# Performance work log

Hardware: AMD Instinct MI355X
Metric: run time of the kernel (lower is better)

The kernel has to match this reference:

```python
import jax, jax.numpy as jnp
import numpy as np

L, ND, ED, AD = 2, 128, 64, 64
N, E, A, G = 50000, 300000, 600000, 16
EPS = 1e-5


def _graph_norm(h, batch, num_graphs, w, b):
    # PyG LayerNorm(mode='graph'): scalar mean/var over all nodes*features per graph.
    F = h.shape[-1]
    cnt = jax.ops.segment_sum(jnp.ones(h.shape[0], h.dtype), batch, num_segments=num_graphs)
    norm = jnp.maximum(cnt, 1.0) * F  # [G]
    mean = (jax.ops.segment_sum(h, batch, num_segments=num_graphs).sum(-1) / norm)[batch][:, None]
    hc = h - mean
    var = (jax.ops.segment_sum(hc * hc, batch, num_segments=num_graphs).sum(-1) / norm)
    out = hc * jax.lax.rsqrt(var + EPS)[batch][:, None]
    return out * w + b


def setup_inputs() -> dict:
    key = jax.random.key(0)
    ks = jax.random.split(key, 24)

    def lin(k, fi, fo):
        return jax.random.normal(k, (L, fi, fo), jnp.float32) / jnp.sqrt(float(fi))

    inp = {
        "x": jax.random.normal(ks[0], (N, ND), jnp.float32),
        "edge_attr": jax.random.normal(ks[1], (E, ED), jnp.float32),
        "angle_attr": jax.random.normal(ks[2], (A, AD), jnp.float32),
        # node_edge_mlp: [2*ND+ED -> ED], plain linear (plain_last=True)
        "W_ne": lin(ks[3], 2 * ND + ED, ED), "b_ne": jnp.zeros((L, ED), jnp.float32),
        "g_e": jnp.ones((L, ED), jnp.float32), "be_e": jnp.zeros((L, ED), jnp.float32),
        # edge_angle_mlp: [2*ED+AD -> AD]
        "W_ea": lin(ks[4], 2 * ED + AD, AD), "b_ea": jnp.zeros((L, AD), jnp.float32),
        "g_a": jnp.ones((L, AD), jnp.float32), "be_a": jnp.zeros((L, AD), jnp.float32),
        # edge_graph_mp message net: [2*ED+AD -> ED]
        "W_emp": lin(ks[5], 2 * ED + AD, ED), "b_emp": jnp.zeros((L, ED), jnp.float32),
        "g_emp": jnp.ones((L, ED), jnp.float32), "be_emp": jnp.zeros((L, ED), jnp.float32),
        # node_graph_mp message net: [2*ND+ED -> ND]
        "W_nmp": lin(ks[6], 2 * ND + ED, ND), "b_nmp": jnp.zeros((L, ND), jnp.float32),
        "g_nmp": jnp.ones((L, ND), jnp.float32), "be_nmp": jnp.zeros((L, ND), jnp.float32),
        "node_batch": jnp.sort(jax.random.randint(ks[7], (N,), 0, G)),
        "edge_index": jax.random.randint(ks[8], (2, E), 0, N),
        "edge_batch": jnp.sort(jax.random.randint(ks[9], (E,), 0, G)),
        "threebody_index": jax.random.randint(ks[10], (2, A), 0, E),
        "angle_batch": jnp.sort(jax.random.randint(ks[11], (A,), 0, G)),
        "num_graphs": G,
    }
    return inp


def reference(x, edge_attr, angle_attr,
              W_ne, b_ne, g_e, be_e,
              W_ea, b_ea, g_a, be_a,
              W_emp, b_emp, g_emp, be_emp,
              W_nmp, b_nmp, g_nmp, be_nmp,
              node_batch, edge_index, edge_batch,
              threebody_index, angle_batch, num_graphs):
    src_e, dst_e = edge_index[0], edge_index[1]
    src_t, dst_t = threebody_index[0], threebody_index[1]
    n_nodes, n_edges = x.shape[0], edge_attr.shape[0]
    for i in range(W_ne.shape[0]):
        # node-pair -> edge update + residual + graph norm
        ecat = jnp.concatenate([x[src_e], x[dst_e], edge_attr], axis=-1)
        edge_attr = edge_attr + ecat @ W_ne[i] + b_ne[i]
        edge_attr = _graph_norm(edge_attr, edge_batch, num_graphs, g_e[i], be_e[i])
        # edge-pair -> angle update + residual + graph norm
        acat = jnp.concatenate([edge_attr[src_t], edge_attr[dst_t], angle_attr], axis=-1)
        angle_attr = angle_attr + acat @ W_ea[i] + b_ea[i]
        angle_attr = _graph_norm(angle_attr, angle_batch, num_graphs, g_a[i], be_a[i])
        # edge_graph_mp: angle-mediated message passing over edges
        mcat = jnp.concatenate([edge_attr[src_t], edge_attr[dst_t], angle_attr], axis=-1)
        msg = jax.nn.relu(mcat @ W_emp[i] + b_emp[i])
        agg = jax.ops.segment_sum(msg, dst_t, num_segments=n_edges)
        edge_attr = _graph_norm(edge_attr + agg, edge_batch, num_graphs, g_emp[i], be_emp[i])
        # node_graph_mp: edge-mediated message passing over nodes
        ncat = jnp.concatenate([x[src_e], x[dst_e], edge_attr], axis=-1)
        nmsg = jax.nn.relu(ncat @ W_nmp[i] + b_nmp[i])
        nagg = jax.ops.segment_sum(nmsg, dst_e, num_segments=n_nodes)
        x = _graph_norm(x + nagg, node_batch, num_graphs, g_nmp[i], be_nmp[i])
    return x
```

## Files before the change

### kernel.cpp

```cpp
#include <hip/hip_runtime.h>

typedef __attribute__((ext_vector_type(8))) short bf16x8_t;
typedef __attribute__((ext_vector_type(4))) short bf16x4_t;
typedef __attribute__((ext_vector_type(4))) float f32x4_t;

constexpr int NG = 16;
constexpr float EPS = 1e-5f;

__device__ inline unsigned short f2bf(float f) {
  unsigned u = __builtin_bit_cast(unsigned, f);
  u += 0x7FFFu + ((u >> 16) & 1u);
  return (unsigned short)(u >> 16);
}
__device__ inline float bf2f(unsigned short u) {
  unsigned x = ((unsigned)u) << 16;
  return __builtin_bit_cast(float, x);
}

__global__ __launch_bounds__(256) void k_dense_x(
    const float* __restrict__ x,
    const unsigned short* __restrict__ WtNE,
    const unsigned short* __restrict__ WtNM,
    unsigned short* __restrict__ P, int nN)
{
  int gw = (int)((blockIdx.x * 256u + threadIdx.x) >> 6);
  int ntile = nN >> 4;
  if (gw >= ntile) return;
  int lane = threadIdx.x & 63;
  int colb = lane & 15;
  int ko = (lane >> 4) << 3;
  int rowb = (lane >> 4) << 2;
  int row = (gw << 4) + colb;
  const float* xr = x + (size_t)row * 128;
  f32x4_t a1[4] = {}, a2[4] = {}, a3[8] = {}, a4[8] = {};
#pragma unroll
  for (int c = 0; c < 4; ++c) {
    float4 f0 = *(const float4*)(xr + c * 32 + ko);
    float4 f1 = *(const float4*)(xr + c * 32 + ko + 4);
    float vv[8] = {f0.x,f0.y,f0.z,f0.w,f1.x,f1.y,f1.z,f1.w};
    bf16x8_t a;
#pragma unroll
    for (int k = 0; k < 8; ++k) a[k] = (short)f2bf(vv[k]);
#pragma unroll
    for (int nb = 0; nb < 4; ++nb) {
      bf16x8_t b1 = *(const bf16x8_t*)(WtNE + (size_t)(nb * 16 + colb) * 320 + c * 32 + ko);
      a1[nb] = __builtin_amdgcn_mfma_f32_16x16x32_bf16(a, b1, a1[nb], 0, 0, 0);
      bf16x8_t b2 = *(const bf16x8_t*)(WtNE + (size_t)(nb * 16 + colb) * 320 + (c + 4) * 32 + ko);
      a2[nb] = __builtin_amdgcn_mfma_f32_16x16x32_bf16(a, b2, a2[nb], 0, 0, 0);
    }
#pragma unroll
    for (int nb = 0; nb < 8; ++nb) {
      bf16x8_t b3 = *(const bf16x8_t*)(WtNM + (size_t)(nb * 16 + colb) * 320 + c * 32 + ko);
      a3[nb] = __builtin_amdgcn_mfma_f32_16x16x32_bf16(a, b3, a3[nb], 0, 0, 0);
      bf16x8_t b4 = *(const bf16x8_t*)(WtNM + (size_t)(nb * 16 + colb) * 320 + (c + 4) * 32 + ko);
      a4[nb] = __builtin_amdgcn_mfma_f32_16x16x32_bf16(a, b4, a4[nb], 0, 0, 0);
    }
  }
#pragma unroll
  for (int r = 0; r < 4; ++r) {
    size_t ro = (size_t)((gw << 4) + rowb + r) * 384;
    bf16x4_t t1, t2;
#pragma unroll
    for (int nb = 0; nb < 4; ++nb) { t1[nb] = (short)f2bf(a1[nb][r]); t2[nb] = (short)f2bf(a2[nb][r]); }
    *(bf16x4_t*)(P + ro + colb * 4) = t1;
    *(bf16x4_t*)(P + ro + 64 + colb * 4) = t2;
    bf16x8_t t3, t4;
#pragma unroll
    for (int nb = 0; nb < 8; ++nb) { t3[nb] = (short)f2bf(a3[nb][r]); t4[nb] = (short)f2bf(a4[nb][r]); }
    *(bf16x8_t*)(P + ro + 128 + colb * 8) = t3;
    *(bf16x8_t*)(P + ro + 256 + colb * 8) = t4;
  }
}

__global__ __launch_bounds__(256) void k_edge(
    const unsigned short* __restrict__ P, const float* e_in, float* e_out,
    const int* __restrict__ ei, const int* __restrict__ ebatch,
    const unsigned short* __restrict__ Wt,
    const float* __restrict__ bias,
    const float* __restrict__ afA, const float* __restrict__ afB,
    float* __restrict__ gs1, float* __restrict__ gs2,
    unsigned short* __restrict__ pn, int nE)
{
  __shared__ float lA[1024], lB[1024];
  __shared__ float ls1[NG], ls2[NG];
  for (int i = threadIdx.x; i < 1024; i += 256) { lA[i] = afA[i]; lB[i] = afB[i]; }
  if (threadIdx.x < NG) { ls1[threadIdx.x] = 0.f; ls2[threadIdx.x] = 0.f; }
  __syncthreads();
  int gw = (int)((blockIdx.x * 256u + threadIdx.x) >> 6);
  int ntile = nE >> 4;
  bool act = gw < ntile;
  int lane = threadIdx.x & 63;
  int colb = lane & 15;
  int ko = (lane >> 4) << 3;
  int rowb = (lane >> 4) << 2;
  float sr[4] = {0.f,0.f,0.f,0.f}, ssr[4] = {0.f,0.f,0.f,0.f};
  if (act) {
    int sI[4], dI[4];
#pragma unroll
    for (int r = 0; r < 4; ++r) {
      int e_r = (gw << 4) + rowb + r;
      sI[r] = ei[e_r]; dI[r] = ei[nE + e_r];
    }
    bf16x4_t g1[4], g2[4]; bf16x8_t g3[4], g4[4];
#pragma unroll
    for (int r = 0; r < 4; ++r) {
      g1[r] = *(const bf16x4_t*)(P + (size_t)sI[r] * 384 + colb * 4);
      g2[r] = *(const bf16x4_t*)(P + (size_t)dI[r] * 384 + 64 + colb * 4);
      g3[r] = *(const bf16x8_t*)(P + (size_t)sI[r] * 384 + 128 + colb * 8);
      g4[r] = *(const bf16x8_t*)(P + (size_t)dI[r] * 384 + 256 + colb * 8);
    }
    int row = (gw << 4) + colb;
    int ge = ebatch[row];
    const float* er = e_in + (size_t)row * 64;
    f32x4_t acc[4] = {};
#pragma unroll
    for (int c2 = 0; c2 < 2; ++c2) {
      int fb = c2 * 32 + ko;
      float4 f0 = *(const float4*)(er + fb);
      float4 f1 = *(const float4*)(er + fb + 4);
      float vv[8] = {f0.x,f0.y,f0.z,f0.w,f1.x,f1.y,f1.z,f1.w};
      bf16x8_t a;
#pragma unroll
      for (int k = 0; k < 8; ++k) a[k] = (short)f2bf(vv[k] * lA[ge*64 + fb + k] + lB[ge*64 + fb + k]);
#pragma unroll
      for (int nb = 0; nb < 4; ++nb) {
        bf16x8_t b = *(const bf16x8_t*)(Wt + (size_t)(nb * 16 + colb) * 320 + (8 + c2) * 32 + ko);
        acc[nb] = __builtin_amdgcn_mfma_f32_16x16x32_bf16(a, b, acc[nb], 0, 0, 0);
      }
    }
#pragma unroll
    for (int r = 0; r < 4; ++r) {
      int e_ = (gw << 4) + rowb + r;
      int gr = ebatch[e_];
#pragma unroll
      for (int nb = 0; nb < 4; ++nb) {
        int col = nb * 16 + colb;
        size_t off = (size_t)e_ * 64 + col;
        float vv = e_in[off] * lA[gr*64 + col] + lB[gr*64 + col] + bias[col]
                 + acc[nb][r] + bf2f((unsigned short)g1[r][nb]) + bf2f((unsigned short)g2[r][nb]);
        e_out[off] = vv;
        sr[r] += vv; ssr[r] += vv * vv;
      }
      bf16x8_t pv;
#pragma unroll
      for (int k = 0; k < 8; ++k)
        pv[k] = (short)f2bf(bf2f((unsigned short)g3[r][k]) + bf2f((unsigned short)g4[r][k]));
      *(bf16x8_t*)(pn + (size_t)e_ * 128 + colb * 8) = pv;
    }
  }
#pragma unroll
  for (int m = 1; m <= 8; m <<= 1)
#pragma unroll
    for (int r = 0; r < 4; ++r) { sr[r] += __shfl_xor(sr[r], m); ssr[r] += __shfl_xor(ssr[r], m); }
  if (act && colb == 0) {
#pragma unroll
    for (int r = 0; r < 4; ++r) {
      int g = ebatch[(gw << 4) + rowb + r];
      atomicAdd(&ls1[g], sr[r]); atomicAdd(&ls2[g], ssr[r]);
    }
  }
  __syncthreads();
  if (threadIdx.x < NG) {
    atomicAdd(&gs1[threadIdx.x], ls1[threadIdx.x]);
    atomicAdd(&gs2[threadIdx.x], ls2[threadIdx.x]);
  }
}

__global__ __launch_bounds__(256) void k_fin_nmp(
    const float* __restrict__ e, const int* __restrict__ ebatch,
    const unsigned short* __restrict__ Wt,
    const float* __restrict__ bias,
    const float* __restrict__ afEA, const float* __restrict__ afEB,
    const unsigned short* __restrict__ pn,
    unsigned short* __restrict__ msg, int nE)
{
  __shared__ float lEA[1024], lEB[1024];
  for (int i = threadIdx.x; i < 1024; i += 256) { lEA[i] = afEA[i]; lEB[i] = afEB[i]; }
  __syncthreads();
  int gw = (int)((blockIdx.x * 256u + threadIdx.x) >> 6);
  int ntile = nE >> 4;
  if (gw >= ntile) return;
  int lane = threadIdx.x & 63;
  int colb = lane & 15;
  int ko = (lane >> 4) << 3;
  int rowb = (lane >> 4) << 2;
  int row = (gw << 4) + colb;
  int ge = ebatch[row];
  const float* er = e + (size_t)row * 64;
  f32x4_t acc[8] = {};
#pragma unroll
  for (int c2 = 0; c2 < 2; ++c2) {
    int fb = c2 * 32 + ko;
    float4 f0 = *(const float4*)(er + fb);
    float4 f1 = *(const float4*)(er + fb + 4);
    float vv[8] = {f0.x,f0.y,f0.z,f0.w,f1.x,f1.y,f1.z,f1.w};
    bf16x8_t a;
#pragma unroll
    for (int k = 0; k < 8; ++k) a[k] = (short)f2bf(vv[k] * lEA[ge*64 + fb + k] + lEB[ge*64 + fb + k]);
#pragma unroll
    for (int nb = 0; nb < 8; ++nb) {
      bf16x8_t b = *(const bf16x8_t*)(Wt + (size_t)(nb * 16 + colb) * 320 + (8 + c2) * 32 + ko);
      acc[nb] = __builtin_amdgcn_mfma_f32_16x16x32_bf16(a, b, acc[nb], 0, 0, 0);
    }
  }
#pragma unroll
  for (int r = 0; r < 4; ++r) {
    int e_ = (gw << 4) + rowb + r;
    bf16x8_t p8 = *(const bf16x8_t*)(pn + (size_t)e_ * 128 + colb * 8);
#pragma unroll
    for (int nb = 0; nb < 8; ++nb) {
      int col = nb * 16 + colb;
      float v = fmaxf(acc[nb][r] + bf2f((unsigned short)p8[nb]) + bias[col], 0.f);
      msg[(size_t)e_ * 128 + col] = f2bf(v);
    }
  }
}

__global__ __launch_bounds__(256) void k_mm_angle(
    const unsigned short* __restrict__ eB1, const float* a_in, float* a_out,
    const int* __restrict__ ti, const int* __restrict__ abatch,
    const unsigned short* __restrict__ Wt, const float* __restrict__ bias,
    const float* __restrict__ afAA, const float* __restrict__ afAB,
    float* __restrict__ gs1, float* __restrict__ gs2, int nA)
{
  __shared__ float lAA[1024], lAB[1024];
  __shared__ float ls1[NG], ls2[NG];
  for (int i = threadIdx.x; i < 1024; i += 256) { lAA[i] = afAA[i]; lAB[i] = afAB[i]; }
  if (threadIdx.x < NG) { ls1[threadIdx.x] = 0.f; ls2[threadIdx.x] = 0.f; }
  __syncthreads();
  int gw = (int)((blockIdx.x * 256u + threadIdx.x) >> 6);
  int ntile = nA >> 4;
  bool act = gw < ntile;
  int lane = threadIdx.x & 63;
  int colb = lane & 15;
  int ko = (lane >> 4) << 3;
  int rowb = (lane >> 4) << 2;
  float sr[4] = {0.f,0.f,0.f,0.f}, ssr[4] = {0.f,0.f,0.f,0.f};
  if (act) {
    int row = (gw << 4) + colb;
    int s = ti[row], d = ti[nA + row];
    int ga = abatch[row];
    const unsigned short* es = eB1 + (size_t)s * 64;
    const unsigned short* ed = eB1 + (size_t)d * 64;
    const float* ar = a_in + (size_t)row * 64;
    f32x4_t acc[4] = {};
#pragma unroll
    for (int c = 0; c < 6; ++c) {
      bf16x8_t a;
      if (c < 4) {
        const unsigned short* bp = (c < 2) ? es + c * 32 : ed + (c - 2) * 32;
        a = *(const bf16x8_t*)(bp + ko);
      } else {
        int fb = (c - 4) * 32 + ko;
        float4 f0 = *(const float4*)(ar + fb);
        float4 f1 = *(const float4*)(ar + fb + 4);
        float vv[8] = {f0.x,f0.y,f0.z,f0.w,f1.x,f1.y,f1.z,f1.w};
#pragma unroll
        for (int k = 0; k < 8; ++k) a[k] = (short)f2bf(vv[k] * lAA[ga*64 + fb + k] + lAB[ga*64 + fb + k]);
      }
#pragma unroll
      for (int nb = 0; nb < 4; ++nb) {
        bf16x8_t b = *(const bf16x8_t*)(Wt + (size_t)(nb * 16 + colb) * 192 + c * 32 + ko);
        acc[nb] = __builtin_amdgcn_mfma_f32_16x16x32_bf16(a, b, acc[nb], 0, 0, 0);
      }
    }
#pragma unroll
    for (int r = 0; r < 4; ++r) {
      int a_ = (gw << 4) + rowb + r;
      int gr = abatch[a_];
#pragma unroll
      for (int nb = 0; nb < 4; ++nb) {
        int col = nb * 16 + colb;
        size_t off = (size_t)a_ * 64 + col;
        float vv = a_in[off] * lAA[gr*64 + col] + lAB[gr*64 + col] + bias[col] + acc[nb][r];
        a_out[off] = vv;
        sr[r] += vv; ssr[r] += vv * vv;
      }
    }
  }
#pragma unroll
  for (int m = 1; m <= 8; m <<= 1)
#pragma unroll
    for (int r = 0; r < 4; ++r) { sr[r] += __shfl_xor(sr[r], m); ssr[r] += __shfl_xor(ssr[r], m); }
  if (act && colb == 0) {
#pragma unroll
    for (int r = 0; r < 4; ++r) {
      int g = abatch[(gw << 4) + rowb + r];
      atomicAdd(&ls1[g], sr[r]); atomicAdd(&ls2[g], ssr[r]);
    }
  }
  __syncthreads();
  if (threadIdx.x < NG) {
    atomicAdd(&gs1[threadIdx.x], ls1[threadIdx.x]);
    atomicAdd(&gs2[threadIdx.x], ls2[threadIdx.x]);
  }
}

__global__ __launch_bounds__(256) void k_mm_emp(
    const unsigned short* __restrict__ eB1, const float* __restrict__ a_,
    const int* __restrict__ ti, const int* __restrict__ abatch,
    const unsigned short* __restrict__ Wt, const float* __restrict__ bias,
    const float* __restrict__ afAA, const float* __restrict__ afAB,
    unsigned short* __restrict__ msg, int nA)
{
  __shared__ float lAA[1024], lAB[1024];
  for (int i = threadIdx.x; i < 1024; i += 256) { lAA[i] = afAA[i]; lAB[i] = afAB[i]; }
  __syncthreads();
  int gw = (int)((blockIdx.x * 256u + threadIdx.x) >> 6);
  int ntile = nA >> 4;
  if (gw >= ntile) return;
  int lane = threadIdx.x & 63;
  int colb = lane & 15;
  int ko = (lane >> 4) << 3;
  int rowb = (lane >> 4) << 2;
  int row = (gw << 4) + colb;
  int s = ti[row], d = ti[nA + row];
  int ga = abatch[row];
  const unsigned short* es = eB1 + (size_t)s * 64;
  const unsigned short* ed = eB1 + (size_t)d * 64;
  const float* ar = a_ + (size_t)row * 64;
  f32x4_t acc[4] = {};
#pragma unroll
  for (int c = 0; c < 6; ++c) {
    bf16x8_t a;
    if (c < 4) {
      const unsigned short* bp = (c < 2) ? es + c * 32 : ed + (c - 2) * 32;
      a = *(const bf16x8_t*)(bp + ko);
    } else {
      int fb = (c - 4) * 32 + ko;
      float4 f0 = *(const float4*)(ar + fb);
      float4 f1 = *(const float4*)(ar + fb + 4);
      float vv[8] = {f0.x,f0.y,f0.z,f0.w,f1.x,f1.y,f1.z,f1.w};
#pragma unroll
      for (int k = 0; k < 8; ++k) a[k] = (short)f2bf(vv[k] * lAA[ga*64 + fb + k] + lAB[ga*64 + fb + k]);
    }
#pragma unroll
    for (int nb = 0; nb < 4; ++nb) {
      bf16x8_t b = *(const bf16x8_t*)(Wt + (size_t)(nb * 16 + colb) * 192 + c * 32 + ko);
      acc[nb] = __builtin_amdgcn_mfma_f32_16x16x32_bf16(a, b, acc[nb], 0, 0, 0);
    }
  }
#pragma unroll
  for (int r = 0; r < 4; ++r) {
    int a_idx = (gw << 4) + rowb + r;
#pragma unroll
    for (int nb = 0; nb < 4; ++nb) {
      int col = nb * 16 + colb;
      float v = fmaxf(acc[nb][r] + bias[col], 0.f);
      msg[(size_t)a_idx * 64 + col] = f2bf(v);
    }
  }
}

__global__ __launch_bounds__(256) void k_red_e(
    const unsigned short* __restrict__ msg, const float* e_in, float* e_out,
    const int* __restrict__ ptr, const int* __restrict__ perm,
    const int* __restrict__ ebatch,
    const float* __restrict__ afA, const float* __restrict__ afB,
    float* __restrict__ gs1, float* __restrict__ gs2, int nE)
{
  __shared__ float lA[1024], lB[1024], ls1[NG], ls2[NG];
  for (int i = threadIdx.x; i < 1024; i += 256) { lA[i] = afA[i]; lB[i] = afB[i]; }
  if (threadIdx.x < NG) { ls1[threadIdx.x] = 0.f; ls2[threadIdx.x] = 0.f; }
  __syncthreads();
  int lane = threadIdx.x & 63;
  int wv = (int)((blockIdx.x * 256u + threadIdx.x) >> 6);
  int nw = (int)((gridDim.x * 256u) >> 6);
  for (int eidx = wv; eidx < nE; eidx += nw) {
    int p0 = ptr[eidx], p1 = ptr[eidx + 1];
    float sum = 0.f;
    for (int j = p0; j < p1; ++j) {
      int aidx = perm[j];
      sum += bf2f(msg[(size_t)aidx * 64 + lane]);
    }
    int g = ebatch[eidx];
    size_t off = (size_t)eidx * 64 + lane;
    float v = e_in[off] * lA[g*64 + lane] + lB[g*64 + lane] + sum;
    e_out[off] = v;
    float s = v, ss = v * v;
#pragma unroll
    for (int m = 1; m < 64; m <<= 1) { s += __shfl_xor(s, m); ss += __shfl_xor(ss, m); }
    if (lane == 0) { atomicAdd(&ls1[g], s); atomicAdd(&ls2[g], ss); }
  }
  __syncthreads();
  if (threadIdx.x < NG) {
    atomicAdd(&gs1[threadIdx.x], ls1[threadIdx.x]);
    atomicAdd(&gs2[threadIdx.x], ls2[threadIdx.x]);
  }
}

__global__ __launch_bounds__(256) void k_red_n(
    const unsigned short* __restrict__ msg, const float* x_in, float* out,
    const int* __restrict__ ptr, const int* __restrict__ perm,
    const int* __restrict__ nbatch,
    float* __restrict__ gs1, float* __restrict__ gs2, int nN)
{
  __shared__ float ls1[NG], ls2[NG];
  if (threadIdx.x < NG) { ls1[threadIdx.x] = 0.f; ls2[threadIdx.x] = 0.f; }
  __syncthreads();
  int lane = threadIdx.x & 63;
  int wv = (int)((blockIdx.x * 256u + threadIdx.x) >> 6);
  int nw = (int)((gridDim.x * 256u) >> 6);
  for (int n = wv; n < nN; n += nw) {
    int p0 = ptr[n], p1 = ptr[n + 1];
    float s0 = 0.f, s1v = 0.f;
    for (int j = p0; j < p1; ++j) {
      int e = perm[j];
      unsigned u = *(const unsigned*)(msg + (size_t)e * 128 + lane * 2);
      s0 += bf2f((unsigned short)(u & 0xffffu));
      s1v += bf2f((unsigned short)(u >> 16));
    }
    size_t off = (size_t)n * 128 + lane * 2;
    float h0 = x_in[off] + s0, h1 = x_in[off + 1] + s1v;
    out[off] = h0; out[off + 1] = h1;
    float s = h0 + h1, ss = h0 * h0 + h1 * h1;
#pragma unroll
    for (int m = 1; m < 64; m <<= 1) { s += __shfl_xor(s, m); ss += __shfl_xor(ss, m); }
    if (lane == 0) { int g = nbatch[n]; atomicAdd(&ls1[g], s); atomicAdd(&ls2[g], ss); }
  }
  __syncthreads();
  if (threadIdx.x < NG) {
    atomicAdd(&gs1[threadIdx.x], ls1[threadIdx.x]);
    atomicAdd(&gs2[threadIdx.x], ls2[threadIdx.x]);
  }
}

__global__ __launch_bounds__(256) void k_mkaff(
    const float* __restrict__ s1, const float* __restrict__ s2,
    const float* __restrict__ cnt, int F,
    const float* __restrict__ w, const float* __restrict__ b,
    float* __restrict__ A, float* __restrict__ B)
{
  int idx = blockIdx.x * 256 + threadIdx.x;
  if (idx >= NG * F) return;
  int g = idx / F, f = idx - g * F;
  float norm = fmaxf(cnt[g], 1.f) * (float)F;
  float m = s1[g] / norm;
  float var = s2[g] / norm - m * m;
  float inv = rsqrtf(var + EPS);
  float a = inv * w[f];
  A[idx] = a;
  B[idx] = b[f] - m * a;
}

__global__ __launch_bounds__(256) void k_idaff(float* __restrict__ A, float* __restrict__ B, int n)
{
  int idx = blockIdx.x * 256 + threadIdx.x;
  if (idx < n) { A[idx] = 1.f; B[idx] = 0.f; }
}

__global__ __launch_bounds__(256) void k_norm_ebf(
    const float* __restrict__ e, const int* __restrict__ ebatch,
    const float* __restrict__ afA, const float* __restrict__ afB,
    unsigned short* __restrict__ eB, int nE)
{
  int total = nE * 8;
  int stride = gridDim.x * 256;
  for (int idx = blockIdx.x * 256 + threadIdx.x; idx < total; idx += stride) {
    int row = idx >> 3, q = (idx & 7) * 8;
    int g = ebatch[row];
    const float* er = e + (size_t)row * 64 + q;
    float4 f0 = *(const float4*)er;
    float4 f1 = *(const float4*)(er + 4);
    float vv[8] = {f0.x,f0.y,f0.z,f0.w,f1.x,f1.y,f1.z,f1.w};
    bf16x8_t o;
#pragma unroll
    for (int k = 0; k < 8; ++k) o[k] = (short)f2bf(vv[k] * afA[g*64 + q + k] + afB[g*64 + q + k]);
    *(bf16x8_t*)(eB + (size_t)row * 64 + q) = o;
  }
}

__global__ __launch_bounds__(256) void k_apply(
    float* h, const int* __restrict__ batch,
    const float* __restrict__ A, const float* __restrict__ B, int nN)
{
  int total = nN * 16;
  int stride = gridDim.x * 256;
  for (int idx = blockIdx.x * 256 + threadIdx.x; idx < total; idx += stride) {
    int row = idx >> 4, q = (idx & 15) * 8;
    int g = batch[row];
    float* hp = h + (size_t)row * 128 + q;
    float4 f0 = *(const float4*)hp;
    float4 f1 = *(const float4*)(hp + 4);
    float vv[8] = {f0.x,f0.y,f0.z,f0.w,f1.x,f1.y,f1.z,f1.w};
#pragma unroll
    for (int k = 0; k < 8; ++k) vv[k] = vv[k] * A[(g << 7) + q + k] + B[(g << 7) + q + k];
    float4 g0 = {vv[0],vv[1],vv[2],vv[3]}, g1 = {vv[4],vv[5],vv[6],vv[7]};
    *(float4*)hp = g0;
    *(float4*)(hp + 4) = g1;
  }
}

__global__ __launch_bounds__(256) void k_count(
    const int* __restrict__ batch, int n, float* __restrict__ cnt)
{
  __shared__ float lc[NG];
  if (threadIdx.x < NG) lc[threadIdx.x] = 0.f;
  __syncthreads();
  for (int i = blockIdx.x * 256 + threadIdx.x; i < n; i += gridDim.x * 256)
    atomicAdd(&lc[batch[i]], 1.f);
  __syncthreads();
  if (threadIdx.x < NG) atomicAdd(&cnt[threadIdx.x], lc[threadIdx.x]);
}

__global__ __launch_bounds__(256) void k_hist(
    const int* __restrict__ dst, int n, int* __restrict__ cnt)
{
  for (int i = blockIdx.x * 256 + threadIdx.x; i < n; i += gridDim.x * 256)
    atomicAdd(&cnt[dst[i]], 1);
}

__global__ __launch_bounds__(256) void k_scan1(
    const int* __restrict__ in, int* __restrict__ out, int* __restrict__ bsum, int n)
{
  __shared__ int wtot[4];
  int tid = threadIdx.x, lane = tid & 63, wid = tid >> 6;
  int base = blockIdx.x * 1024 + tid * 4;
  int v[4];
#pragma unroll
  for (int k = 0; k < 4; ++k) v[k] = (base + k < n) ? in[base + k] : 0;
  int tsum = v[0] + v[1] + v[2] + v[3];
  int incl = tsum;
#pragma unroll
  for (int off = 1; off < 64; off <<= 1) {
    int up = __shfl_up(incl, off);
    if (lane >= off) incl += up;
  }
  if (lane == 63) wtot[wid] = incl;
  __syncthreads();
  if (tid == 0) {
    int r = 0;
#pragma unroll
    for (int w2 = 0; w2 < 4; ++w2) { int t = wtot[w2]; wtot[w2] = r; r += t; }
    bsum[blockIdx.x] = r;
  }
  __syncthreads();
  int excl = wtot[wid] + incl - tsum;
#pragma unroll
  for (int k = 0; k < 4; ++k) {
    if (base + k < n) out[base + k] = excl;
    excl += v[k];
  }
}

__global__ __launch_bounds__(256) void k_scan2(int* __restrict__ bsum, int nb, int* __restrict__ total_out)
{
  __shared__ int wtot[4];
  int tid = threadIdx.x, lane = tid & 63, wid = tid >> 6;
  int base = tid * 4;
  int v[4];
#pragma unroll
  for (int k = 0; k < 4; ++k) v[k] = (base + k < nb) ? bsum[base + k] : 0;
  int tsum = v[0] + v[1] + v[2] + v[3];
  int incl = tsum;
#pragma unroll
  for (int off = 1; off < 64; off <<= 1) {
    int up = __shfl_up(incl, off);
    if (lane >= off) incl += up;
  }
  if (lane == 63) wtot[wid] = incl;
  __syncthreads();
  if (tid == 0) {
    int r = 0;
#pragma unroll
    for (int w2 = 0; w2 < 4; ++w2) { int t = wtot[w2]; wtot[w2] = r; r += t; }
    *total_out = r;
  }
  __syncthreads();
  int excl = wtot[wid] + incl - tsum;
#pragma unroll
  for (int k = 0; k < 4; ++k) {
    if (base + k < nb) bsum[base + k] = excl;
    excl += v[k];
  }
}

__global__ __launch_bounds__(256) void k_scan3(
    int* __restrict__ ptr, int* __restrict__ cur, const int* __restrict__ bsum, int n)
{
  for (int i = blockIdx.x * 256 + threadIdx.x; i < n; i += gridDim.x * 256) {
    int v = ptr[i] + bsum[i >> 10];
    ptr[i] = v; cur[i] = v;
  }
}

__global__ __launch_bounds__(256) void k_scatter(
    const int* __restrict__ dst, int* __restrict__ cur, int* __restrict__ perm, int n)
{
  for (int i = blockIdx.x * 256 + threadIdx.x; i < n; i += gridDim.x * 256) {
    int d = dst[i];
    int p = atomicAdd(&cur[d], 1);
    perm[p] = i;
  }
}

__global__ __launch_bounds__(256) void k_wt(
    const float* __restrict__ W, unsigned short* __restrict__ Wt, int K, int NO)
{
  int idx = blockIdx.x * 256 + threadIdx.x;
  if (idx >= K * NO) return;
  int k = idx / NO, j = idx - k * NO;
  Wt[(size_t)j * K + k] = f2bf(W[idx]);
}

extern "C" void kernel_launch(void* const* d_in, const int* in_sizes, int n_in,
                              void* d_out, int out_size, void* d_ws, size_t ws_size,
                              hipStream_t stream)
{
  const float* x0    = (const float*)d_in[0];
  const float* e0    = (const float*)d_in[1];
  const float* a0    = (const float*)d_in[2];
  const float* W_ne  = (const float*)d_in[3];
  const float* b_ne  = (const float*)d_in[4];
  const float* g_e   = (const float*)d_in[5];
  const float* be_e  = (const float*)d_in[6];
  const float* W_ea  = (const float*)d_in[7];
  const float* b_ea  = (const float*)d_in[8];
  const float* g_a   = (const float*)d_in[9];
  const float* be_a  = (const float*)d_in[10];
  const float* W_emp = (const float*)d_in[11];
  const float* b_emp = (const float*)d_in[12];
  const float* g_emp = (const float*)d_in[13];
  const float* be_emp= (const float*)d_in[14];
  const float* W_nmp = (const float*)d_in[15];
  const float* b_nmp = (const float*)d_in[16];
  const float* g_nmp = (const float*)d_in[17];
  const float* be_nmp= (const float*)d_in[18];
  const int* node_batch  = (const int*)d_in[19];
  const int* edge_index  = (const int*)d_in[20];
  const int* edge_batch  = (const int*)d_in[21];
  const int* tb_index    = (const int*)d_in[22];
  const int* angle_batch = (const int*)d_in[23];

  const int N = in_sizes[0] / 128;
  const int E = in_sizes[1] / 64;
  const int A = in_sizes[2] / 64;

  char* wsp = (char*)d_ws;
  auto alloc = [&](size_t bytes) { char* p = wsp; wsp += (bytes + 255) & ~(size_t)255; return p; };
  float*          eA     = (float*)alloc((size_t)E * 64 * 4);
  float*          aA     = (float*)alloc((size_t)A * 64 * 4);
  unsigned short* msg    = (unsigned short*)alloc((size_t)A * 64 * 2);
  unsigned short* pn     = (unsigned short*)alloc((size_t)E * 128 * 2);
  unsigned short* eB1    = (unsigned short*)alloc((size_t)E * 64 * 2);
  int* ptr_n  = (int*)alloc((size_t)(N + 1) * 4);
  int* cur_n  = (int*)alloc((size_t)N * 4);
  int* perm_n = (int*)alloc((size_t)E * 4);
  int* ptr_e  = (int*)alloc((size_t)(E + 1) * 4);
  int* cur_e  = (int*)alloc((size_t)E * 4);
  int* perm_e = (int*)alloc((size_t)A * 4);
  int* bsum   = (int*)alloc(4096 * 4);
  float* stats = (float*)alloc(5 * NG * 4);
  float* s1    = stats;
  float* s2    = stats + NG;
  float* cnt_n = stats + 2 * NG;
  float* cnt_e = stats + 3 * NG;
  float* cnt_a = stats + 4 * NG;
  float* afE_idA = (float*)alloc(1024 * 4); float* afE_idB = (float*)alloc(1024 * 4);
  float* afA_idA = (float*)alloc(1024 * 4); float* afA_idB = (float*)alloc(1024 * 4);
  float* afE1A   = (float*)alloc(1024 * 4); float* afE1B   = (float*)alloc(1024 * 4);
  float* afE2A   = (float*)alloc(1024 * 4); float* afE2B   = (float*)alloc(1024 * 4);
  float* afA1A   = (float*)alloc(1024 * 4); float* afA1B   = (float*)alloc(1024 * 4);
  float* afXA    = (float*)alloc(2048 * 4); float* afXB    = (float*)alloc(2048 * 4);
  unsigned short* wt_ne  = (unsigned short*)alloc((size_t)2 * 320 * 64 * 2);
  unsigned short* wt_ea  = (unsigned short*)alloc((size_t)2 * 192 * 64 * 2);
  unsigned short* wt_emp = (unsigned short*)alloc((size_t)2 * 192 * 64 * 2);
  unsigned short* wt_nmp = (unsigned short*)alloc((size_t)2 * 320 * 128 * 2);

  unsigned short* P = msg;
  float* x_out = (float*)d_out;

  for (int i = 0; i < 2; ++i) {
    k_wt<<<(320*64 + 255)/256, 256, 0, stream>>>(W_ne  + (size_t)i*320*64,  wt_ne  + (size_t)i*320*64,  320, 64);
    k_wt<<<(192*64 + 255)/256, 256, 0, stream>>>(W_ea  + (size_t)i*192*64,  wt_ea  + (size_t)i*192*64,  192, 64);
    k_wt<<<(192*64 + 255)/256, 256, 0, stream>>>(W_emp + (size_t)i*192*64,  wt_emp + (size_t)i*192*64,  192, 64);
    k_wt<<<(320*128 + 255)/256, 256, 0, stream>>>(W_nmp + (size_t)i*320*128, wt_nmp + (size_t)i*320*128, 320, 128);
  }
  hipMemsetAsync(stats, 0, 5 * NG * 4, stream);
  k_count<<<512, 256, 0, stream>>>(node_batch, N, cnt_n);
  k_count<<<512, 256, 0, stream>>>(edge_batch, E, cnt_e);
  k_count<<<512, 256, 0, stream>>>(angle_batch, A, cnt_a);
  k_idaff<<<4, 256, 0, stream>>>(afE_idA, afE_idB, 1024);
  k_idaff<<<4, 256, 0, stream>>>(afA_idA, afA_idB, 1024);

  hipMemsetAsync(cur_n, 0, (size_t)N * 4, stream);
  hipMemsetAsync(cur_e, 0, (size_t)E * 4, stream);
  k_hist<<<1024, 256, 0, stream>>>(edge_index + E, E, cur_n);
  k_hist<<<1024, 256, 0, stream>>>(tb_index + A, A, cur_e);
  int nbN = (N + 1023) / 1024, nbE = (E + 1023) / 1024;
  k_scan1<<<nbN, 256, 0, stream>>>(cur_n, ptr_n, bsum, N);
  k_scan2<<<1, 256, 0, stream>>>(bsum, nbN, ptr_n + N);
  k_scan3<<<1024, 256, 0, stream>>>(ptr_n, cur_n, bsum, N);
  k_scatter<<<1024, 256, 0, stream>>>(edge_index + E, cur_n, perm_n, E);
  k_scan1<<<nbE, 256, 0, stream>>>(cur_e, ptr_e, bsum, E);
  k_scan2<<<1, 256, 0, stream>>>(bsum, nbE, ptr_e + E);
  k_scan3<<<1024, 256, 0, stream>>>(ptr_e, cur_e, bsum, E);
  k_scatter<<<1024, 256, 0, stream>>>(tb_index + A, cur_e, perm_e, A);

  const float* x_cur = x0;
  int blkE = (E / 16 + 3) / 4;
  int blkA = (A / 16 + 3) / 4;
  int blkN = (N / 16 + 3) / 4;

  for (int i = 0; i < 2; ++i) {
    const float* e_in  = (i == 0) ? e0 : eA;
    const float* a_in  = (i == 0) ? a0 : aA;
    const float* fEinA = (i == 0) ? afE_idA : afE2A;
    const float* fEinB = (i == 0) ? afE_idB : afE2B;
    const float* fAinA = (i == 0) ? afA_idA : afA1A;
    const float* fAinB = (i == 0) ? afA_idB : afA1B;

    k_dense_x<<<blkN, 256, 0, stream>>>(x_cur, wt_ne + (size_t)i*320*64,
                                        wt_nmp + (size_t)i*320*128, P, N);

    hipMemsetAsync(s1, 0, 2 * NG * 4, stream);
    k_edge<<<blkE, 256, 0, stream>>>(P, e_in, eA, edge_index, edge_batch,
                                     wt_ne + (size_t)i*320*64, b_ne + i*64,
                                     fEinA, fEinB, s1, s2, pn, E);
    k_mkaff<<<4, 256, 0, stream>>>(s1, s2, cnt_e, 64, g_e + i*64, be_e + i*64, afE1A, afE1B);
    k_norm_ebf<<<2048, 256, 0, stream>>>(eA, edge_batch, afE1A, afE1B, eB1, E);

    hipMemsetAsync(s1, 0, 2 * NG * 4, stream);
    k_mm_angle<<<blkA, 256, 0, stream>>>(eB1, a_in, aA, tb_index, angle_batch,
                                         wt_ea + (size_t)i*192*64, b_ea + i*64,
                                         fAinA, fAinB, s1, s2, A);
    k_mkaff<<<4, 256, 0, stream>>>(s1, s2, cnt_a, 64, g_a + i*64, be_a + i*64, afA1A, afA1B);

    k_mm_emp<<<blkA, 256, 0, stream>>>(eB1, aA, tb_index, angle_batch,
                                       wt_emp + (size_t)i*192*64, b_emp + i*64,
                                       afA1A, afA1B, msg, A);
    hipMemsetAsync(s1, 0, 2 * NG * 4, stream);
    k_red_e<<<2048, 256, 0, stream>>>(msg, eA, eA, ptr_e, perm_e, edge_batch,
                                      afE1A, afE1B, s1, s2, E);
    k_mkaff<<<4, 256, 0, stream>>>(s1, s2, cnt_e, 64, g_emp + i*64, be_emp + i*64, afE2A, afE2B);

    k_fin_nmp<<<blkE, 256, 0, stream>>>(eA, edge_batch, wt_nmp + (size_t)i*320*128,
                                        b_nmp + i*128, afE2A, afE2B, pn, msg, E);
    hipMemsetAsync(s1, 0, 2 * NG * 4, stream);
    k_red_n<<<2048, 256, 0, stream>>>(msg, x_cur, x_out, ptr_n, perm_n, node_batch,
                                      s1, s2, N);
    k_mkaff<<<8, 256, 0, stream>>>(s1, s2, cnt_n, 128, g_nmp + i*128, be_nmp + i*128, afXA, afXB);
    k_apply<<<2048, 256, 0, stream>>>(x_out, node_batch, afXA, afXB, N);

    x_cur = x_out;
  }
}
```

Baseline: 1.866 ms.

## Precompute per-edge emp projections and gather them in the angle kernel

Splits the edge-angle message matmul by linearity. The edge-feature parts of W_emp are multiplied once per edge (300k rows) into a bf16 PE buffer, instead of once per angle (600k rows). The angle kernel gathers the two projected halves, sums them into the msg buffer, and k_fin_emp adds only the angle-feature projection. This roughly halves the emp matmul work on the edge part and shrinks the gather, but adds an extra workspace buffer plus an intermediate bf16 rounding step, and falls back to the old path if the workspace is too small.

```diff
diff --git a/kernel.cpp b/kernel.cpp
--- a/kernel.cpp
+++ b/kernel.cpp
@@ -72,6 +72,43 @@
   }
 }
 
+__global__ __launch_bounds__(256) void k_dense_e(
+    const unsigned short* __restrict__ eB1,
+    const unsigned short* __restrict__ WtP,
+    unsigned short* __restrict__ PE, int nE)
+{
+  int gw = (int)((blockIdx.x * 256u + threadIdx.x) >> 6);
+  int ntile = nE >> 4;
+  if (gw >= ntile) return;
+  int lane = threadIdx.x & 63;
+  int colb = lane & 15;
+  int ko = (lane >> 4) << 3;
+  int rowb = (lane >> 4) << 2;
+  int row = (gw << 4) + colb;
+  const unsigned short* er = eB1 + (size_t)row * 64;
+  f32x4_t a3[4] = {}, a4[4] = {};
+#pragma unroll
+  for (int c2 = 0; c2 < 2; ++c2) {
+    bf16x8_t a = *(const bf16x8_t*)(er + c2 * 32 + ko);
+#pragma unroll
+    for (int nb = 0; nb < 4; ++nb) {
+      bf16x8_t b3 = *(const bf16x8_t*)(WtP + (size_t)(nb * 16 + colb) * 192 + c2 * 32 + ko);
+      a3[nb] = __builtin_amdgcn_mfma_f32_16x16x32_bf16(a, b3, a3[nb], 0, 0, 0);
+      bf16x8_t b4 = *(const bf16x8_t*)(WtP + (size_t)(nb * 16 + colb) * 192 + 64 + c2 * 32 + ko);
+      a4[nb] = __builtin_amdgcn_mfma_f32_16x16x32_bf16(a, b4, a4[nb], 0, 0, 0);
+    }
+  }
+#pragma unroll
+  for (int r = 0; r < 4; ++r) {
+    size_t ro = (size_t)((gw << 4) + rowb + r) * 128;
+    bf16x4_t t3, t4;
+#pragma unroll
+    for (int nb = 0; nb < 4; ++nb) { t3[nb] = (short)f2bf(a3[nb][r]); t4[nb] = (short)f2bf(a4[nb][r]); }
+    *(bf16x4_t*)(PE + ro + colb * 4) = t3;
+    *(bf16x4_t*)(PE + ro + 64 + colb * 4) = t4;
+  }
+}
+
 __global__ __launch_bounds__(256) void k_edge(
     const unsigned short* __restrict__ P, const float* e_in, float* e_out,
     const int* __restrict__ ei, const int* __restrict__ ebatch,
@@ -163,6 +200,157 @@
   if (threadIdx.x < NG) {
     atomicAdd(&gs1[threadIdx.x], ls1[threadIdx.x]);
     atomicAdd(&gs2[threadIdx.x], ls2[threadIdx.x]);
+  }
+}
+
+__global__ __launch_bounds__(256) void k_angle(
+    const unsigned short* __restrict__ eB1, const unsigned short* __restrict__ PE,
+    const float* a_in, float* a_out,
+    const int* __restrict__ ti, const int* __restrict__ abatch,
+    const unsigned short* __restrict__ Wt, const float* __restrict__ bias,
+    const float* __restrict__ afAA, const float* __restrict__ afAB,
+    float* __restrict__ gs1, float* __restrict__ gs2,
+    unsigned short* __restrict__ pe, int nA)
+{
+  __shared__ float lAA[1024], lAB[1024];
+  __shared__ float ls1[NG], ls2[NG];
+  for (int i = threadIdx.x; i < 1024; i += 256) { lAA[i] = afAA[i]; lAB[i] = afAB[i]; }
+  if (threadIdx.x < NG) { ls1[threadIdx.x] = 0.f; ls2[threadIdx.x] = 0.f; }
+  __syncthreads();
+  int gw = (int)((blockIdx.x * 256u + threadIdx.x) >> 6);
+  int ntile = nA >> 4;
+  bool act = gw < ntile;
+  int lane = threadIdx.x & 63;
+  int colb = lane & 15;
+  int ko = (lane >> 4) << 3;
+  int rowb = (lane >> 4) << 2;
+  float sr[4] = {0.f,0.f,0.f,0.f}, ssr[4] = {0.f,0.f,0.f,0.f};
+  if (act) {
+    int sI[4], dI[4];
+#pragma unroll
+    for (int r = 0; r < 4; ++r) {
+      int a_r = (gw << 4) + rowb + r;
+      sI[r] = ti[a_r]; dI[r] = ti[nA + a_r];
+    }
+    bf16x4_t g3[4], g4[4];
+#pragma unroll
+    for (int r = 0; r < 4; ++r) {
+      g3[r] = *(const bf16x4_t*)(PE + (size_t)sI[r] * 128 + colb * 4);
+      g4[r] = *(const bf16x4_t*)(PE + (size_t)dI[r] * 128 + 64 + colb * 4);
+    }
+    int row = (gw << 4) + colb;
+    int s = ti[row], d = ti[nA + row];
+    int ga = abatch[row];
+    const unsigned short* es = eB1 + (size_t)s * 64;
+    const unsigned short* ed = eB1 + (size_t)d * 64;
+    const float* ar = a_in + (size_t)row * 64;
+    f32x4_t acc[4] = {};
+#pragma unroll
+    for (int c = 0; c < 6; ++c) {
+      bf16x8_t a;
+      if (c < 4) {
+        const unsigned short* bp = (c < 2) ? es + c * 32 : ed + (c - 2) * 32;
+        a = *(const bf16x8_t*)(bp + ko);
+      } else {
+        int fb = (c - 4) * 32 + ko;
+        float4 f0 = *(const float4*)(ar + fb);
+        float4 f1 = *(const float4*)(ar + fb + 4);
+        float vv[8] = {f0.x,f0.y,f0.z,f0.w,f1.x,f1.y,f1.z,f1.w};
+#pragma unroll
+        for (int k = 0; k < 8; ++k) a[k] = (short)f2bf(vv[k] * lAA[ga*64 + fb + k] + lAB[ga*64 + fb + k]);
+      }
+#pragma unroll
+      for (int nb = 0; nb < 4; ++nb) {
+        bf16x8_t b = *(const bf16x8_t*)(Wt + (size_t)(nb * 16 + colb) * 192 + c * 32 + ko);
+        acc[nb] = __builtin_amdgcn_mfma_f32_16x16x32_bf16(a, b, acc[nb], 0, 0, 0);
+      }
+    }
+#pragma unroll
+    for (int r = 0; r < 4; ++r) {
+      int a_ = (gw << 4) + rowb + r;
+      int gr = abatch[a_];
+#pragma unroll
+      for (int nb = 0; nb < 4; ++nb) {
+        int col = nb * 16 + colb;
+        size_t off = (size_t)a_ * 64 + col;
+        float vv = a_in[off] * lAA[gr*64 + col] + lAB[gr*64 + col] + bias[col] + acc[nb][r];
+        a_out[off] = vv;
+        sr[r] += vv; ssr[r] += vv * vv;
+      }
+      bf16x4_t pv;
+#pragma unroll
+      for (int nb = 0; nb < 4; ++nb)
+        pv[nb] = (short)f2bf(bf2f((unsigned short)g3[r][nb]) + bf2f((unsigned short)g4[r][nb]));
+      *(bf16x4_t*)(pe + (size_t)a_ * 64 + colb * 4) = pv;
+    }
+  }
+#pragma unroll
+  for (int m = 1; m <= 8; m <<= 1)
+#pragma unroll
+    for (int r = 0; r < 4; ++r) { sr[r] += __shfl_xor(sr[r], m); ssr[r] += __shfl_xor(ssr[r], m); }
+  if (act && colb == 0) {
+#pragma unroll
+    for (int r = 0; r < 4; ++r) {
+      int g = abatch[(gw << 4) + rowb + r];
+      atomicAdd(&ls1[g], sr[r]); atomicAdd(&ls2[g], ssr[r]);
+    }
+  }
+  __syncthreads();
+  if (threadIdx.x < NG) {
+    atomicAdd(&gs1[threadIdx.x], ls1[threadIdx.x]);
+    atomicAdd(&gs2[threadIdx.x], ls2[threadIdx.x]);
+  }
+}
+
+__global__ __launch_bounds__(256) void k_fin_emp(
+    const float* __restrict__ a_, const int* __restrict__ abatch,
+    const unsigned short* __restrict__ Wt,
+    const float* __restrict__ bias,
+    const float* __restrict__ afAA, const float* __restrict__ afAB,
+    unsigned short* __restrict__ msg, int nA)
+{
+  __shared__ float lAA[1024], lAB[1024];
+  for (int i = threadIdx.x; i < 1024; i += 256) { lAA[i] = afAA[i]; lAB[i] = afAB[i]; }
+  __syncthreads();
+  int gw = (int)((blockIdx.x * 256u + threadIdx.x) >> 6);
+  int ntile = nA >> 4;
+  if (gw >= ntile) return;
+  int lane = threadIdx.x & 63;
+  int colb = lane & 15;
+  int ko = (lane >> 4) << 3;
+  int rowb = (lane >> 4) << 2;
+  int row = (gw << 4) + colb;
+  int ga = abatch[row];
+  const float* ar = a_ + (size_t)row * 64;
+  f32x4_t acc[4] = {};
+#pragma unroll
+  for (int c2 = 0; c2 < 2; ++c2) {
+    int fb = c2 * 32 + ko;
+    float4 f0 = *(const float4*)(ar + fb);
+    float4 f1 = *(const float4*)(ar + fb + 4);
+    float vv[8] = {f0.x,f0.y,f0.z,f0.w,f1.x,f1.y,f1.z,f1.w};
+    bf16x8_t a;
+#pragma unroll
+    for (int k = 0; k < 8; ++k) a[k] = (short)f2bf(vv[k] * lAA[ga*64 + fb + k] + lAB[ga*64 + fb + k]);
+#pragma unroll
+    for (int nb = 0; nb < 4; ++nb) {
+      bf16x8_t b = *(const bf16x8_t*)(Wt + (size_t)(nb * 16 + colb) * 192 + 128 + c2 * 32 + ko);
+      acc[nb] = __builtin_amdgcn_mfma_f32_16x16x32_bf16(a, b, acc[nb], 0, 0, 0);
+    }
+  }
+  bf16x4_t p4[4];
+#pragma unroll
+  for (int r = 0; r < 4; ++r)
+    p4[r] = *(const bf16x4_t*)(msg + (size_t)((gw << 4) + rowb + r) * 64 + colb * 4);
+#pragma unroll
+  for (int r = 0; r < 4; ++r) {
+    int a_idx = (gw << 4) + rowb + r;
+#pragma unroll
+    for (int nb = 0; nb < 4; ++nb) {
+      int col = nb * 16 + colb;
+      float v = fmaxf(acc[nb][r] + bf2f((unsigned short)p4[r][nb]) + bias[col], 0.f);
+      msg[(size_t)a_idx * 64 + col] = f2bf(v);
+    }
   }
 }
 
@@ -666,6 +854,8 @@
   unsigned short* wt_ea  = (unsigned short*)alloc((size_t)2 * 192 * 64 * 2);
   unsigned short* wt_emp = (unsigned short*)alloc((size_t)2 * 192 * 64 * 2);
   unsigned short* wt_nmp = (unsigned short*)alloc((size_t)2 * 320 * 128 * 2);
+  unsigned short* PE     = (unsigned short*)alloc((size_t)E * 128 * 2);
+  bool usePE = ((size_t)(wsp - (char*)d_ws) <= ws_size);
 
   unsigned short* P = msg;
   float* x_out = (float*)d_out;
@@ -720,15 +910,27 @@
     k_mkaff<<<4, 256, 0, stream>>>(s1, s2, cnt_e, 64, g_e + i*64, be_e + i*64, afE1A, afE1B);
     k_norm_ebf<<<2048, 256, 0, stream>>>(eA, edge_batch, afE1A, afE1B, eB1, E);
 
+    if (usePE)
+      k_dense_e<<<blkE, 256, 0, stream>>>(eB1, wt_emp + (size_t)i*192*64, PE, E);
+
     hipMemsetAsync(s1, 0, 2 * NG * 4, stream);
-    k_mm_angle<<<blkA, 256, 0, stream>>>(eB1, a_in, aA, tb_index, angle_batch,
-                                         wt_ea + (size_t)i*192*64, b_ea + i*64,
-                                         fAinA, fAinB, s1, s2, A);
+    if (usePE)
+      k_angle<<<blkA, 256, 0, stream>>>(eB1, PE, a_in, aA, tb_index, angle_batch,
+                                        wt_ea + (size_t)i*192*64, b_ea + i*64,
+                                        fAinA, fAinB, s1, s2, msg, A);
+    else
+      k_mm_angle<<<blkA, 256, 0, stream>>>(eB1, a_in, aA, tb_index, angle_batch,
+                                           wt_ea + (size_t)i*192*64, b_ea + i*64,
+                                           fAinA, fAinB, s1, s2, A);
     k_mkaff<<<4, 256, 0, stream>>>(s1, s2, cnt_a, 64, g_a + i*64, be_a + i*64, afA1A, afA1B);
 
-    k_mm_emp<<<blkA, 256, 0, stream>>>(eB1, aA, tb_index, angle_batch,
-                                       wt_emp + (size_t)i*192*64, b_emp + i*64,
-                                       afA1A, afA1B, msg, A);
+    if (usePE)
+      k_fin_emp<<<blkA, 256, 0, stream>>>(aA, angle_batch, wt_emp + (size_t)i*192*64,
+                                          b_emp + i*64, afA1A, afA1B, msg, A);
+    else
+      k_mm_emp<<<blkA, 256, 0, stream>>>(eB1, aA, tb_index, angle_batch,
+                                         wt_emp + (size_t)i*192*64, b_emp + i*64,
+                                         afA1A, afA1B, msg, A);
     hipMemsetAsync(s1, 0, 2 * NG * 4, stream);
     k_red_e<<<2048, 256, 0, stream>>>(msg, eA, eA, ptr_e, perm_e, edge_batch,
                                       afE1A, afE1B, s1, s2, E);
```

New measurement: 1.840 ms. Within noise of the previous version (-1.4%).
